# Kernel optimization log

Hardware: AMD Instinct MI355X
Metric: run time of the kernel (lower is better)

The kernel has to match this reference:

```python
import math
import jax, jax.numpy as jnp
import numpy as np

B, V, N, D, H = 8, 8, 1000, 256, 8
KS = D // H
TANH_CLIP = 10.0
F_NODE = 8   # node dynamic features incl. is_to_be_delivered flag
F_VEH = 8


def setup_inputs() -> dict:
    key = jax.random.key(0)
    ks = jax.random.split(key, 13)
    s = 1.0 / math.sqrt(D)
    mask = jax.random.uniform(ks[8], (B, V, N)) > 0.3
    mask = mask.at[:, :, 0].set(True)  # guarantee at least one feasible action
    return {
        'node_embeddings': jax.random.normal(ks[0], (B, N, D), jnp.float32),
        'fixed_context': jax.random.normal(ks[1], (B, 1, D), jnp.float32),
        'prev_node_embeddings': jax.random.normal(ks[2], (B, V, D), jnp.float32),
        'node_dynamic_features': jax.random.uniform(ks[3], (B, V, N, F_NODE), jnp.float32),
        'vehicle_dynamic_features': jax.random.uniform(ks[4], (B, V, F_VEH), jnp.float32),
        'glimpse_V_static': jax.random.normal(ks[5], (H, B, 1, N, KS), jnp.float32),
        'glimpse_K_static': jax.random.normal(ks[6], (H, B, 1, N, KS), jnp.float32),
        'logit_K_static': jax.random.normal(ks[7], (B, 1, N, D), jnp.float32),
        'feasibility_mask': mask,
        'pcs_weight': jax.random.normal(ks[9], (D, D + F_VEH), jnp.float32) * s,
        'pns1_weight': jax.random.normal(ks[10], (3 * D, F_NODE - 1), jnp.float32) * s,
        'pns2_weight': jax.random.normal(ks[11], (3 * D, 3 * D + 1), jnp.float32) * s,
        'po_weight': jax.random.normal(ks[12], (D, D), jnp.float32) * s,
    }


def _make_heads(x):
    # [B,V,N,D] -> [H,B,V,N,KS]  (matches unsqueeze/view/permute in torch code)
    b, v, n, _ = x.shape
    return x.reshape(b, v, n, H, KS).transpose(3, 0, 1, 2, 4)


def reference(node_embeddings, fixed_context, prev_node_embeddings,
              node_dynamic_features, vehicle_dynamic_features,
              glimpse_V_static, glimpse_K_static, logit_K_static,
              feasibility_mask, pcs_weight, pns1_weight, pns2_weight, po_weight):
    b, n, d = node_embeddings.shape
    v = vehicle_dynamic_features.shape[1]

    # projected current vehicle state
    cvs = jnp.concatenate([prev_node_embeddings, vehicle_dynamic_features], axis=-1)  # [B,V,D+Fv]
    proj_cvs = cvs @ pcs_weight.T                                                     # [B,V,D]

    # node dynamic embeddings (hypernet linears)
    flag = node_dynamic_features[..., -1:]
    feats = node_dynamic_features[..., :-1]
    x = feats @ pns1_weight.T                                   # [B,V,N,3D]
    x_ = jnp.concatenate([x, flag], axis=-1) @ pns2_weight.T    # [B,V,N,3D]
    nde = x + x_
    gVd, gKd, lKd = jnp.split(nde, 3, axis=-1)                  # each [B,V,N,D]

    glimpse_V = glimpse_V_static + _make_heads(gVd)             # [H,B,V,N,KS]
    glimpse_K = glimpse_K_static + _make_heads(gKd)             # [H,B,V,N,KS]
    logit_K = logit_K_static + lKd                              # [B,V,N,D]

    query = fixed_context + proj_cvs                            # [B,V,D]
    gQ = query.reshape(b, v, H, 1, KS).transpose(2, 0, 1, 3, 4)  # [H,B,V,1,KS]

    logmask = jnp.log(feasibility_mask.astype(jnp.float32))     # 0 / -inf, [B,V,N]

    compat = jnp.einsum('hbvqk,hbvnk->hbvqn', gQ, glimpse_K) / math.sqrt(KS)
    compat = compat + logmask[None, :, :, None, :]              # [H,B,V,1,N]

    # softmax over all (vehicle, node) pairs jointly
    attn = jax.nn.softmax(compat.reshape(H, b, v * n), axis=-1).reshape(compat.shape)
    heads = jnp.einsum('hbvqn,hbvnk->hbvqk', attn, glimpse_V)   # [H,B,V,1,KS]

    concated = heads.transpose(1, 2, 3, 0, 4).reshape(b, v, 1, d)
    final_Q = concated @ po_weight.T                            # [B,V,1,D]

    logits = jnp.einsum('bvqd,bvnd->bvqn', final_Q, logit_K) / math.sqrt(d)
    logits = jnp.tanh(logits) * TANH_CLIP
    logits = logits[:, :, 0, :] + logmask                       # [B,V,N]
    logits = logits.reshape(b, v * n)
    probs = jax.nn.softmax(logits, axis=1)

    # greedy (eval-mode) selection
    op = jnp.argmax(probs, axis=-1)
    prob = jnp.max(probs, axis=-1)
    logprob = jnp.log(prob)
    entropy = -jnp.sum(prob * logprob)
    selected_vecs = (op // n).astype(jnp.int64)
    selected_nodes = op % n
    return selected_vecs, selected_nodes, logprob, entropy
```

## Files before the change

kernel.cpp:

```cpp
#include <hip/hip_runtime.h>
#include <math.h>

#define OFF_MW     0
#define OFF_QUERY  6144
#define OFF_CSUMP  22528
#define OFF_HSTATP 23040
#define OFF_S8P    154112
#define OFF_FQ     186880
#define OFF_LQM    203264
#define OFF_EXPSP  203776
#define OFF_PACKP  204032
#define OFF_DONE   204544
#define OFF_BM     204545

__device__ inline float waveSum(float v){
  #pragma unroll
  for (int o = 32; o > 0; o >>= 1) v += __shfl_down(v, o, 64);
  return v;
}
__device__ inline unsigned long long waveMaxU(unsigned long long v){
  #pragma unroll
  for (int o = 32; o > 0; o >>= 1) {
    unsigned long long w = __shfl_down(v, o, 64);
    v = (w > v) ? w : v;
  }
  return v;
}
__device__ inline unsigned encF(float f){
  unsigned u = __float_as_uint(f);
  return (u & 0x80000000u) ? ~u : (u | 0x80000000u);
}
__device__ inline float decF(unsigned u){
  return (u & 0x80000000u) ? __uint_as_float(u & 0x7fffffffu)
                           : __uint_as_float(~u);
}

__global__ __launch_bounds__(256) void k_prep(
    const float* __restrict__ pns1, const float* __restrict__ pns2,
    const float* __restrict__ prev, const float* __restrict__ veh,
    const float* __restrict__ fixedc, const float* __restrict__ pcs,
    const void* __restrict__ maskp, float* __restrict__ W)
{
  int blk = blockIdx.x, tid = threadIdx.x;
  float* mw     = W + OFF_MW;
  float* queryp = W + OFF_QUERY;

  if (blk < 768) {
    int i = blk;
    __shared__ float red[28];
    const float* row = pns2 + (size_t)i * 769;
    float acc[7] = {0.f,0.f,0.f,0.f,0.f,0.f,0.f};
    #pragma unroll
    for (int t = 0; t < 3; t++) {
      int j = tid + 256 * t;
      float r = row[j];
      const float* w = pns1 + j * 7;
      #pragma unroll
      for (int f = 0; f < 7; f++) acc[f] += r * w[f];
    }
    #pragma unroll
    for (int f = 0; f < 7; f++) {
      float v = waveSum(acc[f]);
      if ((tid & 63) == 0) red[(tid >> 6) * 7 + f] = v;
    }
    __syncthreads();
    if (tid < 7) {
      float s = red[tid] + red[7 + tid] + red[14 + tid] + red[21 + tid];
      mw[i * 8 + tid] = pns1[i * 7 + tid] + s;
    } else if (tid == 7) {
      mw[i * 8 + 7] = row[768];
    }
  } else if (blk < 832) {
    int bv = blk - 768;
    __shared__ __align__(16) float cvs[264];
    cvs[tid] = prev[(size_t)bv * 256 + tid];
    if (tid < 8) cvs[256 + tid] = veh[bv * 8 + tid];
    __syncthreads();
    int b = bv >> 3;
    float a = fixedc[b * 256 + tid];
    const float4* c4 = (const float4*)cvs;
    const float4* w4 = (const float4*)(pcs + (size_t)tid * 264);
    #pragma unroll 4
    for (int k = 0; k < 66; k++) {
      float4 cv = c4[k], wv = w4[k];
      a += cv.x*wv.x + cv.y*wv.y + cv.z*wv.z + cv.w*wv.w;
    }
    queryp[(size_t)bv * 256 + tid] = a;
  } else {
    __shared__ unsigned hits[4];
    const unsigned char* mb = (const unsigned char*)maskp;
    bool hit = (tid > 0) && ((tid & 3) != 0) && (mb[tid] != 0);
    unsigned long long bal = __ballot(hit);
    if ((tid & 63) == 0) hits[tid >> 6] = (bal != 0ull) ? 1u : 0u;
    __syncthreads();
    if (tid == 0) {
      ((unsigned*)(W + OFF_BM))[0] = hits[0] | hits[1] | hits[2] | hits[3];
      ((unsigned*)(W + OFF_DONE))[0] = 0u;
    }
  }
}

__global__ __launch_bounds__(256) void k_attn(
    const float* __restrict__ node_dyn, const float* __restrict__ gVs,
    const float* __restrict__ gKs, const void* __restrict__ maskp,
    float* __restrict__ W)
{
  const int blk = blockIdx.x, tid = threadIdx.x;
  const int b = blk & 7, c = (blk >> 3) & 7, h = blk >> 6;
  const int n0 = c * 125;
  const float* mw     = W + OFF_MW;
  const float* queryp = W + OFF_QUERY;
  float* csum_p  = W + OFF_CSUMP;
  float* hstat_p = W + OFF_HSTATP;
  float* s8_p    = W + OFF_S8P;
  const int bytemode = *(const int*)(W + OFF_BM);

  __shared__ __align__(16) float p[1000];
  __shared__ __align__(16) float gq[256];
  __shared__ float qmk[64];
  __shared__ float red4[4];
  __shared__ float s8part[256];

  gq[tid] = queryp[(size_t)(b * 8 + (tid >> 5)) * 256 + h * 32 + (tid & 31)];
  __syncthreads();
  if (tid < 64) {
    int v = tid >> 3, f = tid & 7;
    float a = 0.f;
    for (int k = 0; k < 32; k++)
      a += gq[v * 32 + k] * mw[(256 + h * 32 + k) * 8 + f];
    qmk[tid] = a;
  }
  __syncthreads();

  float tsum = 0.f;
  for (int e = tid; e < 1000; e += 256) {
    int v = e / 125;
    int n = n0 + (e - v * 125);
    int bvn = (b * 8 + v) * 1000 + n;
    const float4* nd4 = (const float4*)(node_dyn + (size_t)bvn * 8);
    float4 ndA = nd4[0], ndB = nd4[1];
    const float4* gk4 = (const float4*)(gKs + ((size_t)(h * 8 + b) * 1000 + n) * 32);
    const float4* gq4 = (const float4*)(gq + v * 32);
    float s = 0.f;
    #pragma unroll
    for (int k4 = 0; k4 < 8; k4++) {
      float4 g = gk4[k4], q = gq4[k4];
      s += g.x*q.x + g.y*q.y + g.z*q.z + g.w*q.w;
    }
    const float* qm = qmk + v * 8;
    float dyn = ndA.x*qm[0] + ndA.y*qm[1] + ndA.z*qm[2] + ndA.w*qm[3]
              + ndB.x*qm[4] + ndB.y*qm[5] + ndB.z*qm[6] + ndB.w*qm[7];
    bool on = bytemode ? (((const unsigned char*)maskp)[bvn] != 0)
                       : (((const int*)maskp)[bvn] != 0);
    float cc = (s + dyn) * 0.17677669529663687f + (on ? 0.f : -INFINITY);
    float pv = __expf(cc);
    p[e] = pv;
    tsum += pv;
  }
  tsum = waveSum(tsum);
  if ((tid & 63) == 0) red4[tid >> 6] = tsum;
  __syncthreads();
  if (tid == 0) csum_p[blk] = red4[0] + red4[1] + red4[2] + red4[3];
  {
    int v = tid >> 5, k = tid & 31;
    const float* gv = gVs + ((size_t)(h * 8 + b) * 1000 + n0) * 32 + k;
    const float* pr = p + v * 125;
    float a = 0.f;
    #pragma unroll 5
    for (int i = 0; i < 125; i++) a += pr[i] * gv[(size_t)i * 32];
    hstat_p[(size_t)blk * 256 + tid] = a;
  }
  {
    int sidx = tid & 3, vf = tid >> 2;
    int v = vf >> 3, f = vf & 7;
    int i0 = sidx * 32;
    int iN = (sidx == 3) ? 29 : 32;
    const float* nd = node_dyn + ((size_t)(b * 8 + v) * 1000 + n0 + i0) * 8 + f;
    const float* pr = p + v * 125 + i0;
    float a = 0.f;
    for (int i = 0; i < iN; i++) a += pr[i] * nd[i * 8];
    s8part[sidx * 64 + vf] = a;
  }
  __syncthreads();
  if (tid < 64)
    s8_p[(size_t)blk * 64 + tid] = s8part[tid] + s8part[64 + tid]
                                 + s8part[128 + tid] + s8part[192 + tid];
}

__global__ __launch_bounds__(256) void k_fq(
    const float* __restrict__ po, float* __restrict__ W)
{
  const int blk = blockIdx.x, tid = threadIdx.x;
  const int b = blk & 7, v = (blk >> 3) & 7;
  const float* mwgV    = W + OFF_MW;
  const float* mwgL    = W + OFF_MW + 512 * 8;
  const float* csum_p  = W + OFF_CSUMP;
  const float* hstat_p = W + OFF_HSTATP;
  const float* s8_p    = W + OFF_S8P;
  float* fqg  = W + OFF_FQ;
  float* lqmg = W + OFF_LQM;

  __shared__ __align__(16) float hstatF[2048];
  __shared__ float csumF[8];
  __shared__ float s8F[512];
  __shared__ __align__(16) float cl[256];
  __shared__ float fql[256];
  __shared__ float part[256];

  for (int h2 = 0; h2 < 8; h2++) {
    float s = 0.f;
    #pragma unroll
    for (int cc = 0; cc < 8; cc++)
      s += hstat_p[(size_t)((h2 << 6) | (cc << 3) | b) * 256 + tid];
    hstatF[h2 * 256 + tid] = s;
  }
  if (tid < 8) {
    float s = 0.f;
    #pragma unroll
    for (int cc = 0; cc < 8; cc++) s += csum_p[(tid << 6) | (cc << 3) | b];
    csumF[tid] = s;
  }
  for (int idx = tid; idx < 512; idx += 256) {
    int h2 = idx >> 6, vf = idx & 63;
    float s = 0.f;
    #pragma unroll
    for (int cc = 0; cc < 8; cc++)
      s += s8_p[(size_t)((h2 << 6) | (cc << 3) | b) * 64 + vf];
    s8F[idx] = s;
  }
  __syncthreads();
  {
    int h2 = tid >> 5, k2 = tid & 31;
    float dyn = 0.f;
    const float* s8pp = s8F + h2 * 64 + v * 8;
    const float* mwp = mwgV + tid * 8;
    #pragma unroll
    for (int f = 0; f < 8; f++) dyn += s8pp[f] * mwp[f];
    cl[tid] = (hstatF[h2 * 256 + v * 32 + k2] + dyn) / csumF[h2];
  }
  __syncthreads();
  {
    float a = 0.f;
    const float4* c4 = (const float4*)cl;
    const float4* w4 = (const float4*)(po + (size_t)tid * 256);
    #pragma unroll 4
    for (int e = 0; e < 64; e++) {
      float4 cv = c4[e], wv = w4[e];
      a += cv.x*wv.x + cv.y*wv.y + cv.z*wv.z + cv.w*wv.w;
    }
    fql[tid] = a;
    fqg[(size_t)(b * 8 + v) * 256 + tid] = a;
  }
  __syncthreads();
  {
    int cc2 = tid >> 3, f = tid & 7;
    float s = 0.f;
    for (int d = cc2 * 8; d < cc2 * 8 + 8; d++) s += fql[d] * mwgL[d * 8 + f];
    part[tid] = s;
  }
  __syncthreads();
  if (tid < 8) {
    float s = 0.f;
    for (int cc2 = 0; cc2 < 32; cc2++) s += part[cc2 * 8 + tid];
    lqmg[(b * 8 + v) * 8 + tid] = s;
  }
}

__global__ __launch_bounds__(256) void k_logits(
    const float* __restrict__ lKs, const float* __restrict__ node_dyn,
    const void* __restrict__ maskp, float* __restrict__ W,
    float* __restrict__ out)
{
  const int blk = blockIdx.x, tid = threadIdx.x;
  const int b = blk & 7, slice = blk >> 3;
  const int nn = tid >> 3, v = tid & 7;
  const int n = slice * 32 + nn;
  const bool valid = (n < 1000);
  const int n_c = valid ? n : 999;
  const float* fqg  = W + OFF_FQ;
  const float* lqmg = W + OFF_LQM;
  float* expsum_p = W + OFF_EXPSP;
  unsigned long long* packed_p = (unsigned long long*)(W + OFF_PACKP);
  unsigned* done = (unsigned*)(W + OFF_DONE);
  const int bytemode = *(const int*)(W + OFF_BM);

  __shared__ float red4[4];
  __shared__ unsigned long long rP[4];
  __shared__ unsigned ticket;

  int bvn = (b * 8 + v) * 1000 + n_c;
  const float4* A  = (const float4*)(fqg + (size_t)(b * 8 + v) * 256);
  const float4* Bk = (const float4*)(lKs + ((size_t)(b * 1000 + n_c)) * 256);
  float s = 0.f;
  #pragma unroll 8
  for (int d4 = 0; d4 < 64; d4++) {
    float4 x = A[d4], y = Bk[d4];
    s += x.x*y.x + x.y*y.y + x.z*y.z + x.w*y.w;
  }
  const float4* nd4 = (const float4*)(node_dyn + (size_t)bvn * 8);
  float4 na = nd4[0], nb = nd4[1];
  const float* qm = lqmg + (b * 8 + v) * 8;
  float dyn = na.x*qm[0] + na.y*qm[1] + na.z*qm[2] + na.w*qm[3]
            + nb.x*qm[4] + nb.y*qm[5] + nb.z*qm[6] + nb.w*qm[7];
  float z = (s + dyn) * 0.0625f;
  bool on = bytemode ? (((const unsigned char*)maskp)[bvn] != 0)
                     : (((const int*)maskp)[bvn] != 0);
  float L = tanhf(z) * 10.0f + (on ? 0.f : -INFINITY);
  if (!valid) L = -INFINITY;
  float ex = __expf(L);
  unsigned idx = (unsigned)(v * 1000 + n_c);
  unsigned long long pk = ((unsigned long long)encF(L) << 32) | (unsigned)(~idx);
  float sEx = waveSum(ex);
  unsigned long long mP = waveMaxU(pk);
  if ((tid & 63) == 0) { red4[tid >> 6] = sEx; rP[tid >> 6] = mP; }
  __syncthreads();
  if (tid == 0) {
    float S = red4[0] + red4[1] + red4[2] + red4[3];
    unsigned long long P = rP[0];
    #pragma unroll
    for (int i = 1; i < 4; i++) P = (rP[i] > P) ? rP[i] : P;
    atomicExch(&expsum_p[blk], S);
    atomicExch(&packed_p[blk], P);
    __threadfence();
    ticket = atomicAdd(done, 1u);
  }
  __syncthreads();
  if (ticket == 255) {
    __threadfence();
    if (tid < 64) {
      float cEnt = 0.f;
      if (tid < 8) {
        float S = 0.f;
        unsigned long long P = 0ull;
        for (int sl = 0; sl < 32; sl++) {
          int j = sl * 8 + tid;
          S += atomicAdd(&expsum_p[j], 0.0f);
          unsigned long long q = atomicAdd(&packed_p[j], 0ull);
          P = (q > P) ? q : P;
        }
        float best = decF((unsigned)(P >> 32));
        unsigned bi = ~(unsigned)(P & 0xffffffffu);
        float logprob = best - logf(S);
        float prob = __expf(logprob);
        out[tid]      = (float)(bi / 1000);
        out[8 + tid]  = (float)(bi % 1000);
        out[16 + tid] = logprob;
        cEnt = prob * logprob;
      }
      cEnt = waveSum(cEnt);
      if (tid == 0) out[24] = -cEnt;
    }
  }
}

extern "C" void kernel_launch(void* const* d_in, const int* in_sizes, int n_in,
                              void* d_out, int out_size, void* d_ws, size_t ws_size,
                              hipStream_t stream) {
  const float* fixedc   = (const float*)d_in[1];
  const float* prev     = (const float*)d_in[2];
  const float* node_dyn = (const float*)d_in[3];
  const float* veh      = (const float*)d_in[4];
  const float* gVs      = (const float*)d_in[5];
  const float* gKs      = (const float*)d_in[6];
  const float* lKs      = (const float*)d_in[7];
  const void*  mask     = d_in[8];
  const float* pcs      = (const float*)d_in[9];
  const float* pns1     = (const float*)d_in[10];
  const float* pns2     = (const float*)d_in[11];
  const float* po       = (const float*)d_in[12];
  float* W   = (float*)d_ws;
  float* out = (float*)d_out;

  k_prep<<<833, 256, 0, stream>>>(pns1, pns2, prev, veh, fixedc, pcs, mask, W);
  k_attn<<<512, 256, 0, stream>>>(node_dyn, gVs, gKs, mask, W);
  k_fq<<<64, 256, 0, stream>>>(po, W);
  k_logits<<<256, 256, 0, stream>>>(lKs, node_dyn, mask, W, out);
}
```

Baseline: 157.0 us.

## Stage attention and logit operands in shared memory with coalesced loads

In the attention kernel, glimpse V rows, node dynamic features and the mw slice are copied into LDS once and reused from there, replacing strided global reads. In the logits kernel, each block first loads its 32 logit-K rows into padded shared memory cooperatively, so the 8 vehicle threads that need the same row no longer each fetch it from global memory. Several unroll factors are also raised. Shared memory use per block grows a lot (about 52KB in k_attn, about 33KB in k_logits), which can reduce occupancy and adds a barrier before compute.

```diff
diff --git a/kernel.cpp b/kernel.cpp
--- a/kernel.cpp
+++ b/kernel.cpp
@@ -80,7 +80,7 @@
     float a = fixedc[b * 256 + tid];
     const float4* c4 = (const float4*)cvs;
     const float4* w4 = (const float4*)(pcs + (size_t)tid * 264);
-    #pragma unroll 4
+    #pragma unroll 8
     for (int k = 0; k < 66; k++) {
       float4 cv = c4[k], wv = w4[k];
       a += cv.x*wv.x + cv.y*wv.y + cv.z*wv.z + cv.w*wv.w;
@@ -117,18 +117,28 @@
 
   __shared__ __align__(16) float p[1000];
   __shared__ __align__(16) float gq[256];
+  __shared__ float mwK[256];
   __shared__ float qmk[64];
   __shared__ float red4[4];
   __shared__ float s8part[256];
-
-  gq[tid] = queryp[(size_t)(b * 8 + (tid >> 5)) * 256 + h * 32 + (tid & 31)];
+  __shared__ __align__(16) float gvL[4000];
+  __shared__ __align__(16) float ndL[8000];
+
+  gq[tid]  = queryp[(size_t)(b * 8 + (tid >> 5)) * 256 + h * 32 + (tid & 31)];
+  mwK[tid] = mw[(256 + h * 32) * 8 + tid];
   __syncthreads();
   if (tid < 64) {
     int v = tid >> 3, f = tid & 7;
     float a = 0.f;
+    #pragma unroll
     for (int k = 0; k < 32; k++)
-      a += gq[v * 32 + k] * mw[(256 + h * 32 + k) * 8 + f];
+      a += gq[v * 32 + k] * mwK[k * 8 + f];
     qmk[tid] = a;
+  }
+  {
+    const float4* gv4 = (const float4*)(gVs + ((size_t)(h * 8 + b) * 1000 + n0) * 32);
+    float4* d4 = (float4*)gvL;
+    for (int idx = tid; idx < 1000; idx += 256) d4[idx] = gv4[idx];
   }
   __syncthreads();
 
@@ -139,6 +149,8 @@
     int bvn = (b * 8 + v) * 1000 + n;
     const float4* nd4 = (const float4*)(node_dyn + (size_t)bvn * 8);
     float4 ndA = nd4[0], ndB = nd4[1];
+    ((float4*)ndL)[e * 2]     = ndA;
+    ((float4*)ndL)[e * 2 + 1] = ndB;
     const float4* gk4 = (const float4*)(gKs + ((size_t)(h * 8 + b) * 1000 + n) * 32);
     const float4* gq4 = (const float4*)(gq + v * 32);
     float s = 0.f;
@@ -163,11 +175,10 @@
   if (tid == 0) csum_p[blk] = red4[0] + red4[1] + red4[2] + red4[3];
   {
     int v = tid >> 5, k = tid & 31;
-    const float* gv = gVs + ((size_t)(h * 8 + b) * 1000 + n0) * 32 + k;
     const float* pr = p + v * 125;
     float a = 0.f;
     #pragma unroll 5
-    for (int i = 0; i < 125; i++) a += pr[i] * gv[(size_t)i * 32];
+    for (int i = 0; i < 125; i++) a += pr[i] * gvL[i * 32 + k];
     hstat_p[(size_t)blk * 256 + tid] = a;
   }
   {
@@ -175,7 +186,7 @@
     int v = vf >> 3, f = vf & 7;
     int i0 = sidx * 32;
     int iN = (sidx == 3) ? 29 : 32;
-    const float* nd = node_dyn + ((size_t)(b * 8 + v) * 1000 + n0 + i0) * 8 + f;
+    const float* nd = ndL + ((size_t)(v * 125 + i0)) * 8 + f;
     const float* pr = p + v * 125 + i0;
     float a = 0.f;
     for (int i = 0; i < iN; i++) a += pr[i] * nd[i * 8];
@@ -207,6 +218,7 @@
   __shared__ float fql[256];
   __shared__ float part[256];
 
+  #pragma unroll
   for (int h2 = 0; h2 < 8; h2++) {
     float s = 0.f;
     #pragma unroll
@@ -220,6 +232,7 @@
     for (int cc = 0; cc < 8; cc++) s += csum_p[(tid << 6) | (cc << 3) | b];
     csumF[tid] = s;
   }
+  #pragma unroll
   for (int idx = tid; idx < 512; idx += 256) {
     int h2 = idx >> 6, vf = idx & 63;
     float s = 0.f;
@@ -243,7 +256,7 @@
     float a = 0.f;
     const float4* c4 = (const float4*)cl;
     const float4* w4 = (const float4*)(po + (size_t)tid * 256);
-    #pragma unroll 4
+    #pragma unroll 8
     for (int e = 0; e < 64; e++) {
       float4 cv = c4[e], wv = w4[e];
       a += cv.x*wv.x + cv.y*wv.y + cv.z*wv.z + cv.w*wv.w;
@@ -284,13 +297,24 @@
   unsigned* done = (unsigned*)(W + OFF_DONE);
   const int bytemode = *(const int*)(W + OFF_BM);
 
+  __shared__ __align__(16) float bkL[32 * 260];
   __shared__ float red4[4];
   __shared__ unsigned long long rP[4];
   __shared__ unsigned ticket;
 
+  {
+    const float4* src = (const float4*)(lKs + (size_t)b * 1000 * 256);
+    for (int idx = tid; idx < 2048; idx += 256) {
+      int row = idx >> 6, d4 = idx & 63;
+      int ng = slice * 32 + row; if (ng > 999) ng = 999;
+      ((float4*)(bkL + row * 260))[d4] = src[(size_t)ng * 64 + d4];
+    }
+  }
+  __syncthreads();
+
   int bvn = (b * 8 + v) * 1000 + n_c;
   const float4* A  = (const float4*)(fqg + (size_t)(b * 8 + v) * 256);
-  const float4* Bk = (const float4*)(lKs + ((size_t)(b * 1000 + n_c)) * 256);
+  const float4* Bk = (const float4*)(bkL + nn * 260);
   float s = 0.f;
   #pragma unroll 8
   for (int d4 = 0; d4 < 64; d4++) {
```

Result: faster. 146.1 us (-6.9%).
